# Optimization experiments

Hardware: AMD Instinct MI355X
Metric: run time of the kernel (lower is better)

## Reference

```python
import jax, jax.numpy as jnp
import numpy as np
from jax import lax

D_MODEL = 1024
D_STATE = 16
D_CONV = 4
EXPAND = 2
D_INNER = D_MODEL * EXPAND          # 2048
DT_RANK = (D_MODEL + 15) // 16      # 64
B, L = 2, 1024


def setup_inputs() -> dict:
    key = jax.random.key(0)
    ks = jax.random.split(key, 11)
    s = lambda d: 1.0 / np.sqrt(d)
    x = jax.random.normal(ks[0], (B, L, D_MODEL), jnp.float32)
    W_in = jax.random.normal(ks[1], (D_MODEL, 2 * D_INNER), jnp.float32) * s(D_MODEL)
    conv_w = jax.random.normal(ks[2], (D_INNER, D_CONV), jnp.float32) * s(D_CONV)
    conv_b = jax.random.normal(ks[3], (D_INNER,), jnp.float32) * 0.01
    W_x = jax.random.normal(ks[4], (D_INNER, DT_RANK + 2 * D_STATE), jnp.float32) * s(D_INNER)
    W_dt = jax.random.normal(ks[5], (DT_RANK, D_INNER), jnp.float32) * s(DT_RANK)
    # dt bias init as in the torch module: inverse-softplus of dt in [1e-3, 1e-1]
    dt = jnp.exp(jax.random.uniform(ks[6], (D_INNER,), jnp.float32)
                 * (np.log(0.1) - np.log(0.001)) + np.log(0.001))
    dt = jnp.clip(dt, 1e-4, None)
    b_dt = dt + jnp.log(-jnp.expm1(-dt))
    W_out = jax.random.normal(ks[7], (D_INNER, D_MODEL), jnp.float32) * s(D_INNER)
    a = jnp.arange(1, D_STATE + 1, dtype=jnp.float32)[None, :].repeat(D_INNER, axis=0)
    a = a + jax.random.uniform(ks[8], (D_INNER, D_STATE), jnp.float32) * 0.1
    A_log = jnp.log(a)
    D_param = jnp.ones((D_INNER,), jnp.float32)
    return {"x": x, "W_in": W_in, "conv_w": conv_w, "conv_b": conv_b,
            "W_x": W_x, "W_dt": W_dt, "b_dt": b_dt, "W_out": W_out,
            "A_log": A_log, "D_param": D_param}


def _mamba_forward(x, W_in, conv_w, conv_b, W_x, W_dt, b_dt, W_out, A_log, D_param):
    # input projection -> two branches
    xz = x @ W_in                                  # [B,L,2*Di]
    xb, zb = jnp.split(xz, 2, axis=-1)             # each [B,L,Di]
    # causal depthwise conv1d (kernel D_CONV, left pad)
    xp = jnp.pad(xb, ((0, 0), (D_CONV - 1, 0), (0, 0)))
    seq = xb.shape[1]
    xc = conv_b + sum(xp[:, j:j + seq, :] * conv_w[:, j] for j in range(D_CONV))
    u = jax.nn.silu(xc)                            # [B,L,Di]
    # data-dependent SSM parameters
    params = u @ W_x                               # [B,L,dt_rank+2*Ds]
    dlt, b_term, c_term = jnp.split(params, [DT_RANK, DT_RANK + D_STATE], axis=-1)
    delta = jax.nn.softplus(dlt @ W_dt + b_dt)     # [B,L,Di]
    a = -jnp.exp(A_log)                            # [Di,Ds]
    delta_a = jnp.exp(delta[..., None] * a)        # [B,L,Di,Ds]
    delta_b_u = (delta * u)[..., None] * b_term[:, :, None, :]  # [B,L,Di,Ds]

    def step(state, inp):
        da_t, dbu_t, c_t = inp                     # [B,Di,Ds],[B,Di,Ds],[B,Ds]
        state = da_t * state + dbu_t
        y_t = jnp.einsum('bdn,bn->bd', state, c_t)
        return state, y_t

    init = jnp.zeros((x.shape[0], D_INNER, D_STATE), jnp.float32)
    xs = (delta_a.transpose(1, 0, 2, 3),
          delta_b_u.transpose(1, 0, 2, 3),
          c_term.transpose(1, 0, 2))
    _, ys = lax.scan(step, init, xs)               # ys: [L,B,Di]
    y = ys.transpose(1, 0, 2) + D_param * u        # skip term D*u
    y = y * jax.nn.silu(zb)
    return y @ W_out                               # [B,L,Dm]


def reference(x, W_in, conv_w, conv_b, W_x, W_dt, b_dt, W_out, A_log, D_param):
    return _mamba_forward(x, W_in, conv_w, conv_b, W_x, W_dt, b_dt, W_out, A_log, D_param)
```

## Files before the change

### kernel.cpp

```cpp
#include <hip/hip_runtime.h>
#include <hip/hip_bf16.h>
#include <math.h>

#define DM 1024
#define DI 2048
#define DS 16
#define DTR 64
#define NB 2
#define LL 1024
#define MM (NB*LL)
#define NC 32
#define CL (LL/NC)
#define XSPLIT 8
#define XKC (DI/XSPLIT)

typedef unsigned short u16;
typedef __bf16 bf16x8 __attribute__((ext_vector_type(8)));
typedef float f32x4 __attribute__((ext_vector_type(4)));
typedef const __attribute__((address_space(1))) void gas_void;
typedef __attribute__((address_space(3))) void las_void;

__device__ __forceinline__ float sigmoidf_(float x){ return 1.f/(1.f+__expf(-x)); }
__device__ __forceinline__ float siluf_(float x){ return x*sigmoidf_(x); }
__device__ __forceinline__ float softplusf_(float x){ return fmaxf(x,0.f)+__logf(1.f+__expf(-fabsf(x))); }
__device__ __forceinline__ u16 f2b(float f){
  __hip_bfloat16 h = __float2bfloat16(f);
  return __builtin_bit_cast(unsigned short, h);
}
__device__ __forceinline__ size_t smap(size_t i){ return ((i>>11)<<12) + (i&2047); }
__device__ __forceinline__ void gld16(const u16* g, u16* l){
  __builtin_amdgcn_global_load_lds(
      reinterpret_cast<gas_void*>((unsigned long long)g),
      reinterpret_cast<las_void*>((unsigned)(unsigned long long)l), 16, 0, 0);
}

__global__ __launch_bounds__(512) void gemm_mfma_kern(
    const u16* __restrict__ A, const u16* __restrict__ Bt,
    float* __restrict__ C, int M, int N, int lda, int KS, int TN, int TM)
{
  __shared__ __attribute__((aligned(16))) u16 As[128*32];
  __shared__ __attribute__((aligned(16))) u16 Bs[128*32];
  const unsigned t = threadIdx.x;
  const unsigned l = t & 63;
  const unsigned w = t >> 6;
  const unsigned wm = w >> 2, wn = w & 3;
  const int q8  = (int)gridDim.x >> 3;
  const int id2 = ((int)blockIdx.x & 7) * q8 + ((int)blockIdx.x >> 3);
  const int zz  = id2 / (TN*TM);
  const int rr  = id2 % (TN*TM);
  const int bm  = (rr / TN) * 128;
  const int bn  = (rr % TN) * 128;
  const int kbeg = zz * KS;
  const unsigned srow = t >> 2;
  const unsigned scol = (t & 3) * 8;
  f32x4 acc[4][2] = {};
  for (int k0 = kbeg; k0 < kbeg + KS; k0 += 32) {
    gld16(A  + (size_t)(bm + srow)*lda + k0 + scol, As + t*8);
    gld16(Bt + (size_t)(bn + srow)*lda + k0 + scol, Bs + t*8);
    __syncthreads();
    bf16x8 af[4], bfr[2];
    #pragma unroll
    for (int m = 0; m < 4; ++m)
      af[m] = *(const bf16x8*)(As + (wm*64 + m*16 + (l & 15))*32 + (l >> 4)*8);
    #pragma unroll
    for (int n = 0; n < 2; ++n)
      bfr[n] = *(const bf16x8*)(Bs + (wn*32 + n*16 + (l & 15))*32 + (l >> 4)*8);
    #pragma unroll
    for (int m = 0; m < 4; ++m)
      #pragma unroll
      for (int n = 0; n < 2; ++n)
        acc[m][n] = __builtin_amdgcn_mfma_f32_16x16x32_bf16(af[m], bfr[n], acc[m][n], 0, 0, 0);
    __syncthreads();
  }
  float* Cz = C + (size_t)zz*M*N;
  #pragma unroll
  for (int m = 0; m < 4; ++m) {
    #pragma unroll
    for (int n = 0; n < 2; ++n) {
      const int col = bn + wn*32 + n*16 + (l & 15);
      #pragma unroll
      for (int q = 0; q < 4; ++q) {
        const int row = bm + wm*64 + m*16 + (l >> 4)*4 + q;
        Cz[(size_t)row*N + col] = acc[m][n][q];
      }
    }
  }
}

__global__ __launch_bounds__(256) void reduce4_kern(
    const float* __restrict__ part, float* __restrict__ out)
{
  const size_t i = ((size_t)blockIdx.x*256 + threadIdx.x) * 4;
  float4 s = *(const float4*)(part + i);
  #pragma unroll
  for (int ks = 1; ks < 4; ++ks) {
    const float4 v = *(const float4*)(part + (size_t)ks*MM*DM + i);
    s.x+=v.x; s.y+=v.y; s.z+=v.z; s.w+=v.w;
  }
  *(float4*)(out + i) = s;
}

__global__ __launch_bounds__(256) void dtproj_kern(
    const float* __restrict__ params, const float* __restrict__ W_dt,
    const float* __restrict__ b_dt, float* __restrict__ delta)
{
  __shared__ __align__(16) float Ad[32][DTR];
  __shared__ __align__(16) float Wd[DTR][128];
  const int tid = threadIdx.x;
  const int m0 = (blockIdx.x >> 4) * 32;
  const int c0 = (blockIdx.x & 15) * 128;
  #pragma unroll
  for (int i = 0; i < 2; ++i) {
    const int fq = i*256 + tid;
    const int r = fq >> 4, q = fq & 15;
    *(float4*)&Ad[r][q*4] = *(const float4*)(params + (size_t)(m0+r)*96 + q*4);
  }
  #pragma unroll
  for (int i = 0; i < 8; ++i) {
    const int fq = i*256 + tid;
    const int r = fq >> 5, q = fq & 31;
    *(float4*)&Wd[r][q*4] = *(const float4*)(W_dt + (size_t)r*DI + c0 + q*4);
  }
  __syncthreads();
  const int tr = tid >> 5;
  const int tc = tid & 31;
  f32x4 acc[4] = {};
  #pragma unroll
  for (int k0 = 0; k0 < DTR; k0 += 4) {
    float4 a[4], wv[4];
    #pragma unroll
    for (int i = 0; i < 4; ++i) a[i] = *(const float4*)&Ad[tr*4+i][k0];
    #pragma unroll
    for (int j = 0; j < 4; ++j) wv[j] = *(const float4*)&Wd[k0+j][tc*4];
    #pragma unroll
    for (int i = 0; i < 4; ++i) {
      const float ai[4] = {a[i].x, a[i].y, a[i].z, a[i].w};
      #pragma unroll
      for (int j = 0; j < 4; ++j) {
        acc[i][0] = fmaf(ai[j], wv[j].x, acc[i][0]);
        acc[i][1] = fmaf(ai[j], wv[j].y, acc[i][1]);
        acc[i][2] = fmaf(ai[j], wv[j].z, acc[i][2]);
        acc[i][3] = fmaf(ai[j], wv[j].w, acc[i][3]);
      }
    }
  }
  const float4 b4 = *(const float4*)(b_dt + c0 + tc*4);
  #pragma unroll
  for (int i = 0; i < 4; ++i) {
    float4 o;
    o.x = softplusf_(acc[i][0] + b4.x);
    o.y = softplusf_(acc[i][1] + b4.y);
    o.z = softplusf_(acc[i][2] + b4.z);
    o.w = softplusf_(acc[i][3] + b4.w);
    *(float4*)(delta + (size_t)(m0 + tr*4 + i)*DI + c0 + tc*4) = o;
  }
}

__global__ __launch_bounds__(256) void transpose_cvt_kern(
    const float* __restrict__ in, u16* __restrict__ out, int R, int C)
{
  __shared__ float tile[32][33];
  const int r0 = blockIdx.y*32, c0 = blockIdx.x*32;
  const int tr = threadIdx.x >> 3, tc4 = (threadIdx.x & 7) * 4;
  float4 v = *(const float4*)(in + (size_t)(r0+tr)*C + c0 + tc4);
  tile[tr][tc4+0] = v.x; tile[tr][tc4+1] = v.y;
  tile[tr][tc4+2] = v.z; tile[tr][tc4+3] = v.w;
  __syncthreads();
  ushort4 o;
  o.x = f2b(tile[tc4+0][tr]);
  o.y = f2b(tile[tc4+1][tr]);
  o.z = f2b(tile[tc4+2][tr]);
  o.w = f2b(tile[tc4+3][tr]);
  *(ushort4*)(out + (size_t)(c0+tr)*R + r0 + tc4) = o;
}

__global__ __launch_bounds__(256) void cvt_bf16_kern(
    const float* __restrict__ in, int ld, int C, u16* __restrict__ out, int rows)
{
  const int i = blockIdx.x*256 + threadIdx.x;
  if (i >= rows*(C/4)) return;
  const int row = i / (C/4);
  const int cq  = (i % (C/4)) * 4;
  float4 v = *(const float4*)(in + (size_t)row*ld + cq);
  ushort4 o; o.x=f2b(v.x); o.y=f2b(v.y); o.z=f2b(v.z); o.w=f2b(v.w);
  *(ushort4*)(out + (size_t)row*C + cq) = o;
}

__global__ __launch_bounds__(256) void xproj_part_kern(
    const float* __restrict__ u, const float* __restrict__ W_x,
    float* __restrict__ part)
{
  __shared__ __align__(16) float Uk[XKC][32];
  const int tid = threadIdx.x;
  const int m0 = (blockIdx.x & 63) * 32;
  const int ks = blockIdx.x >> 6;
  const int k0 = ks * XKC;
  #pragma unroll
  for (int i = 0; i < 8; ++i) {
    const int fq = i*256 + tid;
    const int r = fq & 31, kq = fq >> 5;
    const float4 v = *(const float4*)(u + (size_t)(m0+r)*DI + k0 + kq*4);
    Uk[kq*4+0][r] = v.x; Uk[kq*4+1][r] = v.y;
    Uk[kq*4+2][r] = v.z; Uk[kq*4+3][r] = v.w;
  }
  __syncthreads();
  const int r4 = tid >> 5;
  const int c  = tid & 31;
  f32x4 a0 = {}, a1 = {}, a2 = {};
  #pragma unroll 4
  for (int k = 0; k < XKC; ++k) {
    const float* w = W_x + (size_t)(k0+k)*96 + c;
    const float w0 = w[0], w1 = w[32], w2 = w[64];
    const float4 uv = *(const float4*)&Uk[k][r4*4];
    const float ur[4] = {uv.x, uv.y, uv.z, uv.w};
    #pragma unroll
    for (int i = 0; i < 4; ++i) {
      a0[i] = fmaf(ur[i], w0, a0[i]);
      a1[i] = fmaf(ur[i], w1, a1[i]);
      a2[i] = fmaf(ur[i], w2, a2[i]);
    }
  }
  #pragma unroll
  for (int i = 0; i < 4; ++i) {
    float* p = part + ((size_t)ks*MM + m0 + r4*4 + i)*96 + c;
    p[0] = a0[i]; p[32] = a1[i]; p[64] = a2[i];
  }
}

__global__ __launch_bounds__(256) void xproj_reduce_kern(
    const float* __restrict__ part, float* __restrict__ params)
{
  const int i = blockIdx.x*256 + threadIdx.x;
  float4 s = {0.f,0.f,0.f,0.f};
  #pragma unroll
  for (int ks = 0; ks < XSPLIT; ++ks) {
    float4 v = *(const float4*)(part + (size_t)ks*MM*96 + (size_t)i*4);
    s.x+=v.x; s.y+=v.y; s.z+=v.z; s.w+=v.w;
  }
  *(float4*)(params + (size_t)i*4) = s;
}

__global__ __launch_bounds__(256) void conv_silu_kern(
    const float* __restrict__ xz, const float* __restrict__ conv_w,
    const float* __restrict__ conv_b, float* __restrict__ u)
{
  const int idx = blockIdx.x * 256 + threadIdx.x;
  const int d4 = (idx & (DI/4 - 1)) * 4;
  const int ml = idx >> 9;
  const int l  = ml & (LL-1);
  const int base = ml - l;
  const float4 w0 = *(const float4*)(conv_w + (d4+0)*4);
  const float4 w1 = *(const float4*)(conv_w + (d4+1)*4);
  const float4 w2 = *(const float4*)(conv_w + (d4+2)*4);
  const float4 w3 = *(const float4*)(conv_w + (d4+3)*4);
  const float wt[4][4] = {{w0.x,w0.y,w0.z,w0.w},{w1.x,w1.y,w1.z,w1.w},
                          {w2.x,w2.y,w2.z,w2.w},{w3.x,w3.y,w3.z,w3.w}};
  float4 acc = *(const float4*)(conv_b + d4);
  #pragma unroll
  for (int j = 0; j < 4; ++j) {
    const int ls = l - 3 + j;
    if (ls >= 0) {
      const float4 v = *(const float4*)(xz + (size_t)(base + ls)*(2*DI) + d4);
      acc.x = fmaf(v.x, wt[0][j], acc.x);
      acc.y = fmaf(v.y, wt[1][j], acc.y);
      acc.z = fmaf(v.z, wt[2][j], acc.z);
      acc.w = fmaf(v.w, wt[3][j], acc.w);
    }
  }
  float4 o;
  o.x = siluf_(acc.x); o.y = siluf_(acc.y);
  o.z = siluf_(acc.z); o.w = siluf_(acc.w);
  *(float4*)(u + (size_t)idx*4) = o;
}

__global__ __launch_bounds__(256) void scan_local_kern(
    const float* __restrict__ delta, const float* __restrict__ u,
    const float* __restrict__ params, const float* __restrict__ A_log,
    float* __restrict__ Pc, float* __restrict__ Fc)
{
  __shared__ __align__(16) float Bs[CL][DS];
  const int flat = blockIdx.x*256 + threadIdx.x;
  const int h  = flat & 1;
  const int ch = flat >> 1;
  const int d = ch & (DI-1);
  const int c = (ch >> 11) & (NC-1);
  const int b = ch >> 16;
  const size_t lbase = (size_t)b*LL + (size_t)c*CL;
  if (threadIdx.x < CL*DS/4) {
    const int row = threadIdx.x >> 2, col4 = (threadIdx.x & 3)*4;
    *(float4*)&Bs[row][col4] = *(const float4*)(params + (lbase+row)*96 + DTR + col4);
  }
  __syncthreads();
  float a[8];
  #pragma unroll
  for (int i = 0; i < 2; ++i) {
    const float4 al = *(const float4*)(A_log + d*DS + h*8 + i*4);
    a[i*4+0] = -expf(al.x); a[i*4+1] = -expf(al.y);
    a[i*4+2] = -expf(al.z); a[i*4+3] = -expf(al.w);
  }
  const float* dl = delta + lbase*DI + d;
  const float* uu = u     + lbase*DI + d;
  float s[8];
  #pragma unroll
  for (int n = 0; n < 8; ++n) s[n] = 0.f;
  float dtsum = 0.f;
  for (int l0 = 0; l0 < CL; l0 += 8) {
    float dtv[8], utv[8];
    #pragma unroll
    for (int j = 0; j < 8; ++j) {
      dtv[j] = dl[(size_t)(l0+j)*DI];
      utv[j] = uu[(size_t)(l0+j)*DI];
    }
    #pragma unroll
    for (int j = 0; j < 8; ++j) {
      const float dt = dtv[j];
      const float dtu = dt*utv[j];
      dtsum += dt;
      const float4 B0 = *(const float4*)&Bs[l0+j][h*8+0];
      const float4 B1 = *(const float4*)&Bs[l0+j][h*8+4];
      const float Bv[8] = {B0.x,B0.y,B0.z,B0.w, B1.x,B1.y,B1.z,B1.w};
      #pragma unroll
      for (int n = 0; n < 8; ++n)
        s[n] = fmaf(__expf(dt*a[n]), s[n], dtu*Bv[n]);
    }
  }
  const size_t base = (((size_t)(b*DI + d))*NC + c)*DS + h*8;
  float4 P0, P1;
  P0.x = __expf(dtsum*a[0]); P0.y = __expf(dtsum*a[1]);
  P0.z = __expf(dtsum*a[2]); P0.w = __expf(dtsum*a[3]);
  P1.x = __expf(dtsum*a[4]); P1.y = __expf(dtsum*a[5]);
  P1.z = __expf(dtsum*a[6]); P1.w = __expf(dtsum*a[7]);
  *(float4*)(Pc + smap(base))     = P0;
  *(float4*)(Pc + smap(base + 4)) = P1;
  *(float4*)(Fc + smap(base))     = make_float4(s[0],s[1],s[2],s[3]);
  *(float4*)(Fc + smap(base + 4)) = make_float4(s[4],s[5],s[6],s[7]);
}

__global__ __launch_bounds__(256) void scan_combine_kern(
    float* __restrict__ PS, const float* __restrict__ Fc)
{
  const int idx = blockIdx.x*256 + threadIdx.x;
  const size_t base = (size_t)(idx >> 4) * (NC*DS) + (idx & 15);
  float s = 0.f;
  #pragma unroll
  for (int c = 0; c < NC; ++c) {
    const size_t a = smap(base + c*DS);
    const float P = PS[a], F = Fc[a];
    PS[a] = s;
    s = fmaf(P, s, F);
  }
}

__global__ __launch_bounds__(256) void scan_apply_kern(
    const float* __restrict__ delta, const float* __restrict__ u,
    const float* __restrict__ params, const float* __restrict__ xz,
    const float* __restrict__ A_log, const float* __restrict__ D_param,
    const float* __restrict__ Sinit, u16* __restrict__ y16)
{
  __shared__ __align__(16) float Bs[CL][DS];
  __shared__ __align__(16) float Cs[CL][DS];
  const int flat = blockIdx.x*256 + threadIdx.x;
  const int h  = flat & 1;
  const int ch = flat >> 1;
  const int d = ch & (DI-1);
  const int c = (ch >> 11) & (NC-1);
  const int b = ch >> 16;
  const size_t lbase = (size_t)b*LL + (size_t)c*CL;
  {
    const int t = threadIdx.x;
    const int row = (t & 127) >> 2, col4 = (t & 3)*4;
    if (t < 128)
      *(float4*)&Bs[row][col4] = *(const float4*)(params + (lbase+row)*96 + DTR + col4);
    else
      *(float4*)&Cs[row][col4] = *(const float4*)(params + (lbase+row)*96 + DTR + DS + col4);
  }
  __syncthreads();
  float a[8];
  #pragma unroll
  for (int i = 0; i < 2; ++i) {
    const float4 al = *(const float4*)(A_log + d*DS + h*8 + i*4);
    a[i*4+0] = -expf(al.x); a[i*4+1] = -expf(al.y);
    a[i*4+2] = -expf(al.z); a[i*4+3] = -expf(al.w);
  }
  const float Dp = D_param[d];
  const float* dl = delta + lbase*DI + d;
  const float* uu = u     + lbase*DI + d;
  const float* zp = xz + lbase*(2*DI) + DI + d;
  u16* yo = y16 + lbase*DI + d;
  const size_t base = (((size_t)(b*DI + d))*NC + c)*DS + h*8;
  float s[8];
  {
    const float4 s0 = *(const float4*)(Sinit + smap(base));
    const float4 s1 = *(const float4*)(Sinit + smap(base + 4));
    s[0]=s0.x; s[1]=s0.y; s[2]=s0.z; s[3]=s0.w;
    s[4]=s1.x; s[5]=s1.y; s[6]=s1.z; s[7]=s1.w;
  }
  for (int l0 = 0; l0 < CL; l0 += 8) {
    float dtv[8], utv[8], zv[8];
    #pragma unroll
    for (int j = 0; j < 8; ++j) {
      dtv[j] = dl[(size_t)(l0+j)*DI];
      utv[j] = uu[(size_t)(l0+j)*DI];
      zv[j]  = zp[(size_t)(l0+j)*(2*DI)];
    }
    u16 yv[8];
    #pragma unroll
    for (int j = 0; j < 8; ++j) {
      const float dt = dtv[j];
      const float ut = utv[j];
      const float dtu = dt*ut;
      const float4 B0 = *(const float4*)&Bs[l0+j][h*8+0];
      const float4 B1 = *(const float4*)&Bs[l0+j][h*8+4];
      const float4 C0 = *(const float4*)&Cs[l0+j][h*8+0];
      const float4 C1 = *(const float4*)&Cs[l0+j][h*8+4];
      const float Bv[8] = {B0.x,B0.y,B0.z,B0.w, B1.x,B1.y,B1.z,B1.w};
      const float Cv[8] = {C0.x,C0.y,C0.z,C0.w, C1.x,C1.y,C1.z,C1.w};
      float part = 0.f;
      #pragma unroll
      for (int n = 0; n < 8; ++n) {
        s[n] = fmaf(__expf(dt*a[n]), s[n], dtu*Bv[n]);
        part = fmaf(s[n], Cv[n], part);
      }
      part += __shfl_xor(part, 1);
      yv[j] = f2b((part + Dp*ut) * siluf_(zv[j]));
    }
    if (h == 0) {
      #pragma unroll
      for (int j = 0; j < 8; ++j)
        yo[(size_t)(l0+j)*DI] = yv[j];
    }
  }
}

extern "C" void kernel_launch(void* const* d_in, const int* in_sizes, int n_in,
                              void* d_out, int out_size, void* d_ws, size_t ws_size,
                              hipStream_t stream)
{
  const float* x      = (const float*)d_in[0];
  const float* W_in   = (const float*)d_in[1];
  const float* conv_w = (const float*)d_in[2];
  const float* conv_b = (const float*)d_in[3];
  const float* W_x    = (const float*)d_in[4];
  const float* W_dt   = (const float*)d_in[5];
  const float* b_dt   = (const float*)d_in[6];
  const float* W_out  = (const float*)d_in[7];
  const float* A_log  = (const float*)d_in[8];
  const float* D_par  = (const float*)d_in[9];
  float* out = (float*)d_out;

  float* xz     = (float*)d_ws;
  float* u      = xz + (size_t)MM*2*DI;
  float* params = u  + (size_t)MM*DI;
  float* delta  = params + (size_t)MM*96;
  u16*  pool    = (u16*)(delta + (size_t)MM*DI);
  u16* xb16 = pool;
  u16* Wi_t = (u16*)out;
  u16* Wo_t   = pool;
  u16* yb16   = pool + (size_t)DM*DI;
  float* xpart = out;
  float* Pc = xz;
  float* Fc = xz + (size_t)1024*4096;
  float* g4part = xz;

  dim3 blk(256);
  dim3 blk512(512);
  cvt_bf16_kern<<<(MM*DM/4 + 255)/256, blk, 0, stream>>>(x, DM, DM, xb16, MM);
  transpose_cvt_kern<<<dim3(2*DI/32, DM/32), blk, 0, stream>>>(W_in, Wi_t, DM, 2*DI);
  gemm_mfma_kern<<<512, blk512, 0, stream>>>(xb16, Wi_t, xz, MM, 2*DI, DM, DM, 32, 16);
  conv_silu_kern<<<(MM*DI/4)/256, blk, 0, stream>>>(xz, conv_w, conv_b, u);
  xproj_part_kern<<<64*XSPLIT, blk, 0, stream>>>(u, W_x, xpart);
  xproj_reduce_kern<<<(MM*96/4)/256, blk, 0, stream>>>(xpart, params);
  dtproj_kern<<<1024, blk, 0, stream>>>(params, W_dt, b_dt, delta);
  scan_local_kern<<<(NB*NC*DI*2)/256, blk, 0, stream>>>(delta, u, params, A_log, Pc, Fc);
  scan_combine_kern<<<(NB*DI*DS)/256, blk, 0, stream>>>(Pc, Fc);
  scan_apply_kern<<<(NB*NC*DI*2)/256, blk, 0, stream>>>(delta, u, params, xz, A_log, D_par, Pc, yb16);
  transpose_cvt_kern<<<dim3(DM/32, DI/32), blk, 0, stream>>>(W_out, Wo_t, DI, DM);
  gemm_mfma_kern<<<512, blk512, 0, stream>>>(yb16, Wo_t, g4part, MM, DM, DI, DI/4, 8, 16);
  reduce4_kern<<<(MM*DM/4)/256, blk, 0, stream>>>(g4part, out);
}
```

Measured before the change: 180.3 us.

## Replace two-pass chunked scan with single recurrence plus elementwise state correction

The chunk-local scan now computes the zero-initialised partial output and the running delta cumsum in one pass, writing them over the delta and u buffers while also emitting the chunk carry terms. A new elementwise finish kernel adds the carried-in state contribution through exp(A*cumsum) times C and the chunk-initial state, then applies the silu(z) gate. This removes the second sequential recurrence over each chunk and replaces it with a parallel per-element pass. A small kernel precomputes -exp(A_log) once. In exchange the finish pass does 16 exps per element, reads a full row of Sinit per element, and the scan writes two extra full-size fp32 arrays.

Measured after the change: 213.5 us. +18.4%, slower.

```diff
diff --git a/kernel.cpp b/kernel.cpp
--- a/kernel.cpp
+++ b/kernel.cpp
@@ -186,6 +186,15 @@
   *(ushort4*)(out + (size_t)row*C + cq) = o;
 }
 
+__global__ __launch_bounds__(256) void negA_kern(
+    const float* __restrict__ A_log, float* __restrict__ negA)
+{
+  const int i = blockIdx.x*256 + threadIdx.x;
+  float4 v = *(const float4*)(A_log + i*4);
+  float4 o; o.x=-expf(v.x); o.y=-expf(v.y); o.z=-expf(v.z); o.w=-expf(v.w);
+  *(float4*)(negA + i*4) = o;
+}
+
 __global__ __launch_bounds__(256) void xproj_part_kern(
     const float* __restrict__ u, const float* __restrict__ W_x,
     float* __restrict__ part)
@@ -273,89 +282,11 @@
   *(float4*)(u + (size_t)idx*4) = o;
 }
 
-__global__ __launch_bounds__(256) void scan_local_kern(
-    const float* __restrict__ delta, const float* __restrict__ u,
-    const float* __restrict__ params, const float* __restrict__ A_log,
+__global__ __launch_bounds__(256) void scan_passA_kern(
+    float* __restrict__ delta, float* __restrict__ u,
+    const float* __restrict__ params, const float* __restrict__ negA,
+    const float* __restrict__ D_param,
     float* __restrict__ Pc, float* __restrict__ Fc)
-{
-  __shared__ __align__(16) float Bs[CL][DS];
-  const int flat = blockIdx.x*256 + threadIdx.x;
-  const int h  = flat & 1;
-  const int ch = flat >> 1;
-  const int d = ch & (DI-1);
-  const int c = (ch >> 11) & (NC-1);
-  const int b = ch >> 16;
-  const size_t lbase = (size_t)b*LL + (size_t)c*CL;
-  if (threadIdx.x < CL*DS/4) {
-    const int row = threadIdx.x >> 2, col4 = (threadIdx.x & 3)*4;
-    *(float4*)&Bs[row][col4] = *(const float4*)(params + (lbase+row)*96 + DTR + col4);
-  }
-  __syncthreads();
-  float a[8];
-  #pragma unroll
-  for (int i = 0; i < 2; ++i) {
-    const float4 al = *(const float4*)(A_log + d*DS + h*8 + i*4);
-    a[i*4+0] = -expf(al.x); a[i*4+1] = -expf(al.y);
-    a[i*4+2] = -expf(al.z); a[i*4+3] = -expf(al.w);
-  }
-  const float* dl = delta + lbase*DI + d;
-  const float* uu = u     + lbase*DI + d;
-  float s[8];
-  #pragma unroll
-  for (int n = 0; n < 8; ++n) s[n] = 0.f;
-  float dtsum = 0.f;
-  for (int l0 = 0; l0 < CL; l0 += 8) {
-    float dtv[8], utv[8];
-    #pragma unroll
-    for (int j = 0; j < 8; ++j) {
-      dtv[j] = dl[(size_t)(l0+j)*DI];
-      utv[j] = uu[(size_t)(l0+j)*DI];
-    }
-    #pragma unroll
-    for (int j = 0; j < 8; ++j) {
-      const float dt = dtv[j];
-      const float dtu = dt*utv[j];
-      dtsum += dt;
-      const float4 B0 = *(const float4*)&Bs[l0+j][h*8+0];
-      const float4 B1 = *(const float4*)&Bs[l0+j][h*8+4];
-      const float Bv[8] = {B0.x,B0.y,B0.z,B0.w, B1.x,B1.y,B1.z,B1.w};
-      #pragma unroll
-      for (int n = 0; n < 8; ++n)
-        s[n] = fmaf(__expf(dt*a[n]), s[n], dtu*Bv[n]);
-    }
-  }
-  const size_t base = (((size_t)(b*DI + d))*NC + c)*DS + h*8;
-  float4 P0, P1;
-  P0.x = __expf(dtsum*a[0]); P0.y = __expf(dtsum*a[1]);
-  P0.z = __expf(dtsum*a[2]); P0.w = __expf(dtsum*a[3]);
-  P1.x = __expf(dtsum*a[4]); P1.y = __expf(dtsum*a[5]);
-  P1.z = __expf(dtsum*a[6]); P1.w = __expf(dtsum*a[7]);
-  *(float4*)(Pc + smap(base))     = P0;
-  *(float4*)(Pc + smap(base + 4)) = P1;
-  *(float4*)(Fc + smap(base))     = make_float4(s[0],s[1],s[2],s[3]);
-  *(float4*)(Fc + smap(base + 4)) = make_float4(s[4],s[5],s[6],s[7]);
-}
-
-__global__ __launch_bounds__(256) void scan_combine_kern(
-    float* __restrict__ PS, const float* __restrict__ Fc)
-{
-  const int idx = blockIdx.x*256 + threadIdx.x;
-  const size_t base = (size_t)(idx >> 4) * (NC*DS) + (idx & 15);
-  float s = 0.f;
-  #pragma unroll
-  for (int c = 0; c < NC; ++c) {
-    const size_t a = smap(base + c*DS);
-    const float P = PS[a], F = Fc[a];
-    PS[a] = s;
-    s = fmaf(P, s, F);
-  }
-}
-
-__global__ __launch_bounds__(256) void scan_apply_kern(
-    const float* __restrict__ delta, const float* __restrict__ u,
-    const float* __restrict__ params, const float* __restrict__ xz,
-    const float* __restrict__ A_log, const float* __restrict__ D_param,
-    const float* __restrict__ Sinit, u16* __restrict__ y16)
 {
   __shared__ __align__(16) float Bs[CL][DS];
   __shared__ __align__(16) float Cs[CL][DS];
@@ -376,39 +307,32 @@
   }
   __syncthreads();
   float a[8];
-  #pragma unroll
-  for (int i = 0; i < 2; ++i) {
-    const float4 al = *(const float4*)(A_log + d*DS + h*8 + i*4);
-    a[i*4+0] = -expf(al.x); a[i*4+1] = -expf(al.y);
-    a[i*4+2] = -expf(al.z); a[i*4+3] = -expf(al.w);
+  {
+    const float4 a0 = *(const float4*)(negA + d*DS + h*8);
+    const float4 a1 = *(const float4*)(negA + d*DS + h*8 + 4);
+    a[0]=a0.x; a[1]=a0.y; a[2]=a0.z; a[3]=a0.w;
+    a[4]=a1.x; a[5]=a1.y; a[6]=a1.z; a[7]=a1.w;
   }
   const float Dp = D_param[d];
-  const float* dl = delta + lbase*DI + d;
-  const float* uu = u     + lbase*DI + d;
-  const float* zp = xz + lbase*(2*DI) + DI + d;
-  u16* yo = y16 + lbase*DI + d;
-  const size_t base = (((size_t)(b*DI + d))*NC + c)*DS + h*8;
+  float* dl = delta + lbase*DI + d;
+  float* uu = u     + lbase*DI + d;
   float s[8];
-  {
-    const float4 s0 = *(const float4*)(Sinit + smap(base));
-    const float4 s1 = *(const float4*)(Sinit + smap(base + 4));
-    s[0]=s0.x; s[1]=s0.y; s[2]=s0.z; s[3]=s0.w;
-    s[4]=s1.x; s[5]=s1.y; s[6]=s1.z; s[7]=s1.w;
-  }
+  #pragma unroll
+  for (int n = 0; n < 8; ++n) s[n] = 0.f;
+  float cum = 0.f;
   for (int l0 = 0; l0 < CL; l0 += 8) {
-    float dtv[8], utv[8], zv[8];
+    float dtv[8], utv[8];
     #pragma unroll
     for (int j = 0; j < 8; ++j) {
       dtv[j] = dl[(size_t)(l0+j)*DI];
       utv[j] = uu[(size_t)(l0+j)*DI];
-      zv[j]  = zp[(size_t)(l0+j)*(2*DI)];
-    }
-    u16 yv[8];
+    }
+    float pav[8], cumv[8];
     #pragma unroll
     for (int j = 0; j < 8; ++j) {
       const float dt = dtv[j];
-      const float ut = utv[j];
-      const float dtu = dt*ut;
+      const float dtu = dt*utv[j];
+      cum += dt; cumv[j] = cum;
       const float4 B0 = *(const float4*)&Bs[l0+j][h*8+0];
       const float4 B1 = *(const float4*)&Bs[l0+j][h*8+4];
       const float4 C0 = *(const float4*)&Cs[l0+j][h*8+0];
@@ -422,14 +346,72 @@
         part = fmaf(s[n], Cv[n], part);
       }
       part += __shfl_xor(part, 1);
-      yv[j] = f2b((part + Dp*ut) * siluf_(zv[j]));
+      pav[j] = part + Dp*utv[j];
     }
     if (h == 0) {
       #pragma unroll
-      for (int j = 0; j < 8; ++j)
-        yo[(size_t)(l0+j)*DI] = yv[j];
-    }
-  }
+      for (int j = 0; j < 8; ++j) {
+        dl[(size_t)(l0+j)*DI] = pav[j];
+        uu[(size_t)(l0+j)*DI] = cumv[j];
+      }
+    }
+  }
+  const size_t base = (((size_t)(b*DI + d))*NC + c)*DS + h*8;
+  float4 P0, P1;
+  P0.x = __expf(cum*a[0]); P0.y = __expf(cum*a[1]);
+  P0.z = __expf(cum*a[2]); P0.w = __expf(cum*a[3]);
+  P1.x = __expf(cum*a[4]); P1.y = __expf(cum*a[5]);
+  P1.z = __expf(cum*a[6]); P1.w = __expf(cum*a[7]);
+  *(float4*)(Pc + smap(base))     = P0;
+  *(float4*)(Pc + smap(base + 4)) = P1;
+  *(float4*)(Fc + smap(base))     = make_float4(s[0],s[1],s[2],s[3]);
+  *(float4*)(Fc + smap(base + 4)) = make_float4(s[4],s[5],s[6],s[7]);
+}
+
+__global__ __launch_bounds__(256) void scan_combine_kern(
+    float* __restrict__ PS, const float* __restrict__ Fc)
+{
+  const int idx = blockIdx.x*256 + threadIdx.x;
+  const size_t base = (size_t)(idx >> 4) * (NC*DS) + (idx & 15);
+  float s = 0.f;
+  #pragma unroll
+  for (int c = 0; c < NC; ++c) {
+    const size_t a = smap(base + c*DS);
+    const float P = PS[a], F = Fc[a];
+    PS[a] = s;
+    s = fmaf(P, s, F);
+  }
+}
+
+__global__ __launch_bounds__(256) void scan_finish_kern(
+    const float* __restrict__ partA, const float* __restrict__ cum,
+    const float* __restrict__ params, const float* __restrict__ xz,
+    const float* __restrict__ negA, const float* __restrict__ Sinit,
+    u16* __restrict__ y16)
+{
+  const int idx = blockIdx.x*256 + threadIdx.x;
+  const int d  = idx & (DI-1);
+  const int ml = idx >> 11;
+  const int l  = ml & (LL-1);
+  const int b  = ml >> 10;
+  const int c  = l >> 5;
+  const float pA = partA[idx];
+  const float cm = cum[idx];
+  const float z  = xz[(size_t)ml*(2*DI) + DI + d];
+  const float* Cr = params + (size_t)ml*96 + DTR + DS;
+  const size_t base = (((size_t)(b*DI + d))*NC + c)*DS;
+  float acc = pA;
+  #pragma unroll
+  for (int i = 0; i < 4; ++i) {
+    const float4 a4 = *(const float4*)(negA + d*DS + i*4);
+    const float4 S4 = *(const float4*)(Sinit + smap(base + i*4));
+    const float4 C4 = *(const float4*)(Cr + i*4);
+    acc = fmaf(C4.x*__expf(a4.x*cm), S4.x, acc);
+    acc = fmaf(C4.y*__expf(a4.y*cm), S4.y, acc);
+    acc = fmaf(C4.z*__expf(a4.z*cm), S4.z, acc);
+    acc = fmaf(C4.w*__expf(a4.w*cm), S4.w, acc);
+  }
+  y16[idx] = f2b(acc * siluf_(z));
 }
 
 extern "C" void kernel_launch(void* const* d_in, const int* in_sizes, int n_in,
@@ -458,6 +440,7 @@
   u16* Wo_t   = pool;
   u16* yb16   = pool + (size_t)DM*DI;
   float* xpart = out;
+  float* negA  = out + (size_t)1800*1024;
   float* Pc = xz;
   float* Fc = xz + (size_t)1024*4096;
   float* g4part = xz;
@@ -470,10 +453,11 @@
   conv_silu_kern<<<(MM*DI/4)/256, blk, 0, stream>>>(xz, conv_w, conv_b, u);
   xproj_part_kern<<<64*XSPLIT, blk, 0, stream>>>(u, W_x, xpart);
   xproj_reduce_kern<<<(MM*96/4)/256, blk, 0, stream>>>(xpart, params);
+  negA_kern<<<(DI*DS/4)/256, blk, 0, stream>>>(A_log, negA);
   dtproj_kern<<<1024, blk, 0, stream>>>(params, W_dt, b_dt, delta);
-  scan_local_kern<<<(NB*NC*DI*2)/256, blk, 0, stream>>>(delta, u, params, A_log, Pc, Fc);
+  scan_passA_kern<<<(NB*NC*DI*2)/256, blk, 0, stream>>>(delta, u, params, negA, D_par, Pc, Fc);
   scan_combine_kern<<<(NB*DI*DS)/256, blk, 0, stream>>>(Pc, Fc);
-  scan_apply_kern<<<(NB*NC*DI*2)/256, blk, 0, stream>>>(delta, u, params, xz, A_log, D_par, Pc, yb16);
+  scan_finish_kern<<<(MM*DI)/256, blk, 0, stream>>>(delta, u, params, xz, negA, Pc, yb16);
   transpose_cvt_kern<<<dim3(DM/32, DI/32), blk, 0, stream>>>(W_out, Wo_t, DI, DM);
   gemm_mfma_kern<<<512, blk512, 0, stream>>>(yb16, Wo_t, g4part, MM, DM, DI, DI/4, 8, 16);
   reduce4_kern<<<(MM*DM/4)/256, blk, 0, stream>>>(g4part, out);
```
